# Performance work log

Hardware: AMD Instinct MI355X
Metric: run time of the kernel (lower is better)

Reference implementation:

```python
import jax, jax.numpy as jnp
import numpy as np

UNITS = 512
EPS = 1e-6

def setup_inputs() -> dict:
    key = jax.random.key(0)
    x = jax.random.normal(key, (262144, UNITS), dtype=jnp.float32)
    return {"x": x}

def reference(x):
    d = x.shape[1]
    # Gram matrix with diagonal jitter: [d, d]
    g = x.T @ x + jnp.eye(d, dtype=x.dtype) * EPS
    L = jnp.linalg.cholesky(g)  # lower triangular [d, d]
    # inv(L) via triangular solve (same math as tf.linalg.inv on L)
    L_inv = jax.scipy.linalg.solve_triangular(L, jnp.eye(d, dtype=x.dtype), lower=True)
    ortho_weights = L_inv.T * jnp.sqrt(jnp.float32(UNITS))
    return x @ ortho_weights
```

## Files before the change

kernel.cpp:

```cpp
#include <hip/hip_runtime.h>


#define EPSJ 1e-6f
#define SQRTD 22.627416997969522f

typedef short bf16x8 __attribute__((ext_vector_type(8)));
typedef float f32x4 __attribute__((ext_vector_type(4)));

__device__ __forceinline__ unsigned short f2bf(float f) {
  unsigned u = __float_as_uint(f);
  unsigned r = u + 0x7fffu + ((u >> 16) & 1u);
  return (unsigned short)(r >> 16);
}

__device__ __forceinline__ int swz(int row, int slot) {
  return slot ^ ((row ^ (row >> 3)) & 7);
}

__device__ __forceinline__ float wred(float s) {
  s += __shfl_xor(s, 1);  s += __shfl_xor(s, 2);  s += __shfl_xor(s, 4);
  s += __shfl_xor(s, 8);  s += __shfl_xor(s, 16); s += __shfl_xor(s, 32);
  return s;
}

#define GLOAD16(g, l)                                                         \
  __builtin_amdgcn_global_load_lds(                                           \
      (const __attribute__((address_space(1))) void*)(g),                     \
      (__attribute__((address_space(3))) void*)(l), 16, 0, 0)

__global__ void convert_bf(const float* __restrict__ X,
                           unsigned short* __restrict__ Xbf) {
  long idx = (long)blockIdx.x * blockDim.x + threadIdx.x;
  const long stride = (long)gridDim.x * blockDim.x;
  const long nch = 134217728 / 8;
  for (long i = idx; i < nch; i += stride) {
    float4 f0 = ((const float4*)X)[i * 2];
    float4 f1 = ((const float4*)X)[i * 2 + 1];
    uint4 o;
    o.x = (unsigned)f2bf(f0.x) | ((unsigned)f2bf(f0.y) << 16);
    o.y = (unsigned)f2bf(f0.z) | ((unsigned)f2bf(f0.w) << 16);
    o.z = (unsigned)f2bf(f1.x) | ((unsigned)f2bf(f1.y) << 16);
    o.w = (unsigned)f2bf(f1.z) | ((unsigned)f2bf(f1.w) << 16);
    ((uint4*)Xbf)[i] = o;
  }
}

__device__ __forceinline__ void stage_pack4(
    const unsigned short* __restrict__ src,
    unsigned short* dst, int c0, int kg) {
  uint4 r0 = *(const uint4*)src;
  uint4 r1 = *(const uint4*)(src + 512);
  uint4 r2 = *(const uint4*)(src + 1024);
  uint4 r3 = *(const uint4*)(src + 1536);
  unsigned a[4] = {r0.x, r0.y, r0.z, r0.w};
  unsigned b[4] = {r1.x, r1.y, r1.z, r1.w};
  unsigned c[4] = {r2.x, r2.y, r2.z, r2.w};
  unsigned d[4] = {r3.x, r3.y, r3.z, r3.w};
  const int khi = kg >> 1, koff = (kg & 1) * 8;
  #pragma unroll
  for (int s = 0; s < 8; ++s) {
    int wsel = s >> 1, sh = (s & 1) * 16;
    unsigned v0 = (a[wsel] >> sh) & 0xFFFFu;
    unsigned v1 = (b[wsel] >> sh) & 0xFFFFu;
    unsigned v2 = (c[wsel] >> sh) & 0xFFFFu;
    unsigned v3 = (d[wsel] >> sh) & 0xFFFFu;
    int cc = c0 + s;
    int sl = khi ^ ((cc ^ (cc >> 3)) & 7);
    *(uint2*)((char*)dst + cc * 128 + sl * 16 + koff) =
        make_uint2(v0 | (v1 << 16), v2 | (v3 << 16));
  }
}

__global__ __launch_bounds__(512, 2) void gram_bf(
    const unsigned short* __restrict__ Xbf, float* __restrict__ part,
    int nchunk) {
  __shared__ unsigned short As[256 * 64];
  __shared__ unsigned short Bs[256 * 64];
  const int b = blockIdx.x, pos = b % 3, chunk = b / 3;
  const int s0 = (int)((long)4096 * chunk / nchunk);
  const int s1 = (int)((long)4096 * (chunk + 1) / nchunk);
  const int ca = (pos == 1) ? 256 : 0;
  const int cb2 = (pos == 0) ? 0 : 256;
  const bool diag = (pos != 2);
  const int t = threadIdx.x, lane = t & 63, w = t >> 6;
  const int wr = w >> 2, wc = w & 3;

  f32x4 acc[8][4];
  const f32x4 zf = {0.f, 0.f, 0.f, 0.f};
  #pragma unroll
  for (int a = 0; a < 8; ++a)
    #pragma unroll
    for (int bb = 0; bb < 4; ++bb) acc[a][bb] = zf;

  const int c0 = (t & 31) * 8;
  const int kg = t >> 5;

  for (int ks = s0; ks < s1; ++ks) {
    long r = (long)ks * 64 + kg * 4;
    stage_pack4(Xbf + r * 512 + ca + c0, As, c0, kg);
    if (!diag) stage_pack4(Xbf + r * 512 + cb2 + c0, Bs, c0, kg);
    __syncthreads();
    const unsigned short* Bp = diag ? As : Bs;
    #pragma unroll
    for (int kk = 0; kk < 2; ++kk) {
      bf16x8 af[8], bfr[4];
      #pragma unroll
      for (int fm = 0; fm < 8; ++fm) {
        int row = wr * 128 + fm * 16 + (lane & 15);
        int slot = swz(row, kk * 4 + (lane >> 4));
        af[fm] = *(const bf16x8*)((const char*)As + row * 128 + slot * 16);
      }
      #pragma unroll
      for (int fn = 0; fn < 4; ++fn) {
        int row = wc * 64 + fn * 16 + (lane & 15);
        int slot = swz(row, kk * 4 + (lane >> 4));
        bfr[fn] = *(const bf16x8*)((const char*)Bp + row * 128 + slot * 16);
      }
      #pragma unroll
      for (int fm = 0; fm < 8; ++fm)
        #pragma unroll
        for (int fn = 0; fn < 4; ++fn)
          acc[fm][fn] = __builtin_amdgcn_mfma_f32_16x16x32_bf16(
              bfr[fn], af[fm], acc[fm][fn], 0, 0, 0);
    }
    __syncthreads();
  }
  float* out = part + (long)b * 65536;
  #pragma unroll
  for (int fm = 0; fm < 8; ++fm)
    #pragma unroll
    for (int fn = 0; fn < 4; ++fn) {
      int mi = wr * 128 + fm * 16 + (lane & 15);
      int nj = wc * 64 + fn * 16 + (lane >> 4) * 4;
      *(float4*)(out + mi * 256 + nj) = *(float4*)&acc[fm][fn];
    }
}

__global__ __launch_bounds__(512, 2) void gram_f32(
    const float* __restrict__ X, float* __restrict__ part, int nchunk) {
  __shared__ unsigned short As[256 * 64];
  __shared__ unsigned short Bs[256 * 64];
  const int b = blockIdx.x;
  const int pos = b % 3;
  const int chunk = b / 3;
  const int CR = 262144 / nchunk;
  const long r0 = (long)chunk * CR;
  const int ca = (pos == 1) ? 256 : 0;
  const int cb = (pos == 0) ? 0 : 256;
  const bool diag = (pos != 2);
  const int t = threadIdx.x, lane = t & 63, w = t >> 6;
  const int wr = w >> 2, wc = w & 3;

  f32x4 acc[8][4];
  const f32x4 zf = {0.f, 0.f, 0.f, 0.f};
  #pragma unroll
  for (int a = 0; a < 8; ++a)
    #pragma unroll
    for (int bb = 0; bb < 4; ++bb) acc[a][bb] = zf;

  const int c_oct = t & 31, msub = t >> 5;

  for (int ks = 0; ks < CR; ks += 64) {
    #pragma unroll
    for (int it = 0; it < 4; ++it) {
      int m = msub + 16 * it;
      long row = r0 + ks + m;
      const float4* sa = (const float4*)(X + row * 512 + ca + c_oct * 8);
      float4 a0 = sa[0], a1 = sa[1];
      {
        float v[8] = {a0.x, a0.y, a0.z, a0.w, a1.x, a1.y, a1.z, a1.w};
        #pragma unroll
        for (int s = 0; s < 8; ++s) {
          int c = c_oct * 8 + s;
          int off = c * 128 + ((2 * m) ^ (((c ^ (c >> 3)) & 7) << 4));
          *(unsigned short*)((char*)As + off) = f2bf(v[s]);
        }
      }
      if (!diag) {
        const float4* sb = (const float4*)(X + row * 512 + cb + c_oct * 8);
        float4 b0 = sb[0], b1 = sb[1];
        float v[8] = {b0.x, b0.y, b0.z, b0.w, b1.x, b1.y, b1.z, b1.w};
        #pragma unroll
        for (int s = 0; s < 8; ++s) {
          int c = c_oct * 8 + s;
          int off = c * 128 + ((2 * m) ^ (((c ^ (c >> 3)) & 7) << 4));
          *(unsigned short*)((char*)Bs + off) = f2bf(v[s]);
        }
      }
    }
    __syncthreads();
    const unsigned short* Bp = diag ? As : Bs;
    #pragma unroll
    for (int kk = 0; kk < 2; ++kk) {
      bf16x8 af[8], bfr[4];
      #pragma unroll
      for (int fm = 0; fm < 8; ++fm) {
        int row = wr * 128 + fm * 16 + (lane & 15);
        int slot = swz(row, kk * 4 + (lane >> 4));
        af[fm] = *(const bf16x8*)((const char*)As + row * 128 + slot * 16);
      }
      #pragma unroll
      for (int fn = 0; fn < 4; ++fn) {
        int row = wc * 64 + fn * 16 + (lane & 15);
        int slot = swz(row, kk * 4 + (lane >> 4));
        bfr[fn] = *(const bf16x8*)((const char*)Bp + row * 128 + slot * 16);
      }
      #pragma unroll
      for (int fm = 0; fm < 8; ++fm)
        #pragma unroll
        for (int fn = 0; fn < 4; ++fn)
          acc[fm][fn] = __builtin_amdgcn_mfma_f32_16x16x32_bf16(
              af[fm], bfr[fn], acc[fm][fn], 0, 0, 0);
    }
    __syncthreads();
  }
  float* out = part + (long)b * 65536;
  #pragma unroll
  for (int fm = 0; fm < 8; ++fm)
    #pragma unroll
    for (int fn = 0; fn < 4; ++fn)
      #pragma unroll
      for (int j = 0; j < 4; ++j) {
        int i  = wr * 128 + fm * 16 + (lane >> 4) * 4 + j;
        int jj = wc * 64 + fn * 16 + (lane & 15);
        out[i * 256 + jj] = acc[fm][fn][j];
      }
}

__global__ void gram_reduce(const float* __restrict__ part,
                            float* __restrict__ G, int nchunk) {
  int idx = blockIdx.x * 256 + threadIdx.x;
  int pos = idx >> 16;
  int e = idx & 65535;
  float s = 0.f;
  for (int ch = 0; ch < nchunk; ++ch)
    s += part[(long)(ch * 3 + pos) * 65536 + e];
  int i = e >> 8, j = e & 255;
  if (pos == 0) {
    G[i * 512 + j] = s;
  } else if (pos == 1) {
    G[(256 + i) * 512 + 256 + j] = s;
  } else {
    G[i * 512 + 256 + j] = s;
    G[(256 + j) * 512 + i] = s;
  }
}

__global__ __launch_bounds__(256) void chol_d64(float* __restrict__ G,
                                                float* __restrict__ Dinv,
                                                int p) {
  __shared__ float Pb[64][65];
  __shared__ float Sb[64][65];
  __shared__ float Inv[64][65];
  __shared__ float Tt[32][33];
  const int t = threadIdx.x;
  const int r0 = 64 * p;
  const int tr = (t >> 4) * 4, tc = (t & 15) * 4;

  for (int idx = t; idx < 4096; idx += 256) {
    int i = idx >> 6, j = idx & 63;
    float v = G[(long)(r0 + i) * 512 + r0 + j];
    if (i == j) v += EPSJ;
    Pb[i][j] = v;
  }
  __syncthreads();

  if (p > 0) {
    float cc[4][4] = {{0.f}};
    for (int r = 0; r < p; ++r) {
      for (int idx = t; idx < 4096; idx += 256) {
        int i = idx >> 6, j = idx & 63;
        Sb[i][j] = G[(long)(r0 + i) * 512 + 64 * r + j];
      }
      __syncthreads();
      #pragma unroll 4
      for (int k = 0; k < 64; ++k) {
        float a0 = Sb[tr][k], a1 = Sb[tr+1][k], a2 = Sb[tr+2][k], a3 = Sb[tr+3][k];
        float b0 = Sb[tc][k], b1 = Sb[tc+1][k], b2 = Sb[tc+2][k], b3 = Sb[tc+3][k];
        cc[0][0]+=a0*b0; cc[0][1]+=a0*b1; cc[0][2]+=a0*b2; cc[0][3]+=a0*b3;
        cc[1][0]+=a1*b0; cc[1][1]+=a1*b1; cc[1][2]+=a1*b2; cc[1][3]+=a1*b3;
        cc[2][0]+=a2*b0; cc[2][1]+=a2*b1; cc[2][2]+=a2*b2; cc[2][3]+=a2*b3;
        cc[3][0]+=a3*b0; cc[3][1]+=a3*b1; cc[3][2]+=a3*b2; cc[3][3]+=a3*b3;
      }
      __syncthreads();
    }
    #pragma unroll
    for (int u = 0; u < 4; ++u)
      #pragma unroll
      for (int v = 0; v < 4; ++v)
        Pb[tr + u][tc + v] -= cc[u][v];
    __syncthreads();
  }

  const int lane = t & 63, w = t >> 6;
  #pragma unroll
  for (int sp = 0; sp < 2; ++sp) {
    const int b0 = sp * 32;
    if (w == 0) {
      float rr[32];
      #pragma unroll
      for (int k = 0; k < 32; ++k)
        rr[k] = (lane < 32) ? Pb[b0 + lane][b0 + k] : 0.f;
      #pragma unroll
      for (int j = 0; j < 32; ++j) {
        float d = sqrtf(__shfl(rr[j], j));
        if (lane == j) rr[j] = d;
        else if (lane > j && lane < 32) rr[j] = rr[j] / d;
        float rj = rr[j];
        #pragma unroll
        for (int k = j + 1; k < 32; ++k) {
          float Lkj = __shfl(rj, k);
          if (lane > j && lane < 32) rr[k] -= rj * Lkj;
        }
      }
      #pragma unroll
      for (int k = 0; k < 32; ++k)
        if (lane < 32) Pb[b0 + lane][b0 + k] = rr[k];
    }
    __syncthreads();
    if (sp == 0) {
      if (t < 32) {
        int rw = 32 + t;
        float x[32];
        #pragma unroll
        for (int j = 0; j < 32; ++j) x[j] = Pb[rw][j];
        #pragma unroll
        for (int j = 0; j < 32; ++j) {
          float xj = x[j] / Pb[j][j];
          x[j] = xj;
          #pragma unroll
          for (int k2 = j + 1; k2 < 32; ++k2) x[k2] -= xj * Pb[k2][j];
        }
        #pragma unroll
        for (int j = 0; j < 32; ++j) Pb[rw][j] = x[j];
      }
      __syncthreads();
      {
        int i = 32 + (t >> 3), kb = 32 + (t & 7) * 4;
        float sv[4];
        #pragma unroll
        for (int e = 0; e < 4; ++e) sv[e] = Pb[i][kb + e];
        #pragma unroll 4
        for (int j = 0; j < 32; ++j) {
          float aij = Pb[i][j];
          #pragma unroll
          for (int e = 0; e < 4; ++e) sv[e] -= aij * Pb[kb + e][j];
        }
        #pragma unroll
        for (int e = 0; e < 4; ++e) Pb[i][kb + e] = sv[e];
      }
      __syncthreads();
    }
  }

  if (t < 64) {
    int col = t & 31, o = (t >> 5) * 32;
    float x[32];
    #pragma unroll
    for (int i = 0; i < 32; ++i) {
      float s = (i == col) ? 1.f : 0.f;
      #pragma unroll
      for (int j = 0; j < i; ++j) s -= Pb[o + i][o + j] * x[j];
      x[i] = s / Pb[o + i][o + i];
    }
    #pragma unroll
    for (int i = 0; i < 32; ++i) Inv[o + i][o + col] = x[i];
  }
  for (int idx = t; idx < 1024; idx += 256)
    Inv[idx >> 5][32 + (idx & 31)] = 0.f;
  __syncthreads();
  {
    int i = t >> 3, jb = (t & 7) * 4;
    float sv[4] = {0.f, 0.f, 0.f, 0.f};
    #pragma unroll 4
    for (int k = 0; k < 32; ++k) {
      float bik = Pb[32 + i][k];
      #pragma unroll
      for (int e = 0; e < 4; ++e) sv[e] += bik * Inv[k][jb + e];
    }
    #pragma unroll
    for (int e = 0; e < 4; ++e) Tt[i][jb + e] = sv[e];
  }
  __syncthreads();
  {
    int i = t >> 3, jb = (t & 7) * 4;
    float sv[4] = {0.f, 0.f, 0.f, 0.f};
    #pragma unroll 4
    for (int k = 0; k < 32; ++k) {
      float cik = Inv[32 + i][32 + k];
      #pragma unroll
      for (int e = 0; e < 4; ++e) sv[e] += cik * Tt[k][jb + e];
    }
    #pragma unroll
    for (int e = 0; e < 4; ++e) Inv[32 + i][jb + e] = -sv[e];
  }
  __syncthreads();
  for (int idx = t; idx < 4096; idx += 256) {
    int i = idx >> 6, j = idx & 63;
    G[(long)(r0 + i) * 512 + r0 + j] = Pb[i][j];
    Dinv[p * 4096 + idx] = Inv[i][j];
  }
}

__global__ __launch_bounds__(256) void chol_t64(float* __restrict__ G,
                                                const float* __restrict__ Dinv,
                                                int p) {
  __shared__ float SbI[64][65];
  __shared__ float SbP[64][65];
  __shared__ float Ub[64][65];
  __shared__ float Db[64][65];
  const int t = threadIdx.x;
  const long rI = 64 * (p + 1 + blockIdx.x), cP = 64 * p;
  const int tr = (t >> 4) * 4, tc = (t & 15) * 4;

  for (int idx = t; idx < 4096; idx += 256)
    Db[idx >> 6][idx & 63] = Dinv[p * 4096 + idx];

  float cc[4][4] = {{0.f}};
  for (int r = 0; r < p; ++r) {
    __syncthreads();
    for (int idx = t; idx < 4096; idx += 256) {
      int i = idx >> 6, j = idx & 63;
      SbI[i][j] = G[(rI + i) * 512 + 64 * r + j];
      SbP[i][j] = G[(cP + i) * 512 + 64 * r + j];
    }
    __syncthreads();
    #pragma unroll 4
    for (int k = 0; k < 64; ++k) {
      float a0 = SbI[tr][k], a1 = SbI[tr+1][k], a2 = SbI[tr+2][k], a3 = SbI[tr+3][k];
      float b0 = SbP[tc][k], b1 = SbP[tc+1][k], b2 = SbP[tc+2][k], b3 = SbP[tc+3][k];
      cc[0][0]+=a0*b0; cc[0][1]+=a0*b1; cc[0][2]+=a0*b2; cc[0][3]+=a0*b3;
      cc[1][0]+=a1*b0; cc[1][1]+=a1*b1; cc[1][2]+=a1*b2; cc[1][3]+=a1*b3;
      cc[2][0]+=a2*b0; cc[2][1]+=a2*b1; cc[2][2]+=a2*b2; cc[2][3]+=a2*b3;
      cc[3][0]+=a3*b0; cc[3][1]+=a3*b1; cc[3][2]+=a3*b2; cc[3][3]+=a3*b3;
    }
  }
  __syncthreads();
  #pragma unroll
  for (int u = 0; u < 4; ++u)
    #pragma unroll
    for (int v = 0; v < 4; ++v)
      Ub[tr + u][tc + v] =
          G[(rI + tr + u) * 512 + cP + tc + v] - cc[u][v];
  __syncthreads();
  float xx[4][4] = {{0.f}};
  #pragma unroll 4
  for (int k = 0; k < 64; ++k) {
    float a0 = Ub[tr][k], a1 = Ub[tr+1][k], a2 = Ub[tr+2][k], a3 = Ub[tr+3][k];
    float b0 = Db[tc][k], b1 = Db[tc+1][k], b2 = Db[tc+2][k], b3 = Db[tc+3][k];
    xx[0][0]+=a0*b0; xx[0][1]+=a0*b1; xx[0][2]+=a0*b2; xx[0][3]+=a0*b3;
    xx[1][0]+=a1*b0; xx[1][1]+=a1*b1; xx[1][2]+=a1*b2; xx[1][3]+=a1*b3;
    xx[2][0]+=a2*b0; xx[2][1]+=a2*b1; xx[2][2]+=a2*b2; xx[2][3]+=a2*b3;
    xx[3][0]+=a3*b0; xx[3][1]+=a3*b1; xx[3][2]+=a3*b2; xx[3][3]+=a3*b3;
  }
  #pragma unroll
  for (int u = 0; u < 4; ++u)
    #pragma unroll
    for (int v = 0; v < 4; ++v)
      G[(rI + tr + u) * 512 + cP + tc + v] = xx[u][v];
}

__global__ __launch_bounds__(256) void tri_assemble(
    const float* __restrict__ G, const float* __restrict__ Dinv,
    unsigned short* __restrict__ Wt) {
  __shared__ float Bsh[448 * 64];
  __shared__ float T[64 * 64];
  const int q = blockIdx.x, t = threadIdx.x;
  const int or_ = (t >> 4) * 4, oc = (t & 15) * 4;

  for (int p = q + 1; p < 8; ++p) {
    float cc[4][4] = {{0.f}};
    for (int r = q; r < p; ++r) {
      const float* Lbase = G + (long)(64 * p) * 512 + 64 * r;
      #pragma unroll 4
      for (int k = 0; k < 64; ++k) {
        float a0 = Lbase[(or_ + 0) * 512 + k];
        float a1 = Lbase[(or_ + 1) * 512 + k];
        float a2 = Lbase[(or_ + 2) * 512 + k];
        float a3 = Lbase[(or_ + 3) * 512 + k];
        float b0, b1, b2, b3;
        if (r == q) {
          const float* Bq = Dinv + q * 4096 + k * 64 + oc;
          b0 = Bq[0]; b1 = Bq[1]; b2 = Bq[2]; b3 = Bq[3];
        } else {
          const float* Br = Bsh + ((r - q - 1) * 64 + k) * 64 + oc;
          b0 = Br[0]; b1 = Br[1]; b2 = Br[2]; b3 = Br[3];
        }
        cc[0][0] += a0*b0; cc[0][1] += a0*b1; cc[0][2] += a0*b2; cc[0][3] += a0*b3;
        cc[1][0] += a1*b0; cc[1][1] += a1*b1; cc[1][2] += a1*b2; cc[1][3] += a1*b3;
        cc[2][0] += a2*b0; cc[2][1] += a2*b1; cc[2][2] += a2*b2; cc[2][3] += a2*b3;
        cc[3][0] += a3*b0; cc[3][1] += a3*b1; cc[3][2] += a3*b2; cc[3][3] += a3*b3;
      }
    }
    #pragma unroll
    for (int u = 0; u < 4; ++u)
      #pragma unroll
      for (int v = 0; v < 4; ++v)
        T[(or_ + u) * 64 + oc + v] = cc[u][v];
    __syncthreads();

    float c2[4][4] = {{0.f}};
    const float* Dp = Dinv + p * 4096;
    #pragma unroll 4
    for (int k = 0; k < 64; ++k) {
      float a0 = Dp[(or_ + 0) * 64 + k];
      float a1 = Dp[(or_ + 1) * 64 + k];
      float a2 = Dp[(or_ + 2) * 64 + k];
      float a3 = Dp[(or_ + 3) * 64 + k];
      const float* Tk = T + k * 64 + oc;
      float b0 = Tk[0], b1 = Tk[1], b2 = Tk[2], b3 = Tk[3];
      c2[0][0] += a0*b0; c2[0][1] += a0*b1; c2[0][2] += a0*b2; c2[0][3] += a0*b3;
      c2[1][0] += a1*b0; c2[1][1] += a1*b1; c2[1][2] += a1*b2; c2[1][3] += a1*b3;
      c2[2][0] += a2*b0; c2[2][1] += a2*b1; c2[2][2] += a2*b2; c2[2][3] += a2*b3;
      c2[3][0] += a3*b0; c2[3][1] += a3*b1; c2[3][2] += a3*b2; c2[3][3] += a3*b3;
    }
    #pragma unroll
    for (int u = 0; u < 4; ++u)
      #pragma unroll
      for (int v = 0; v < 4; ++v)
        Bsh[((p - q - 1) * 64 + or_ + u) * 64 + oc + v] = -c2[u][v];
    __syncthreads();
  }

  const int nr = (8 - q) * 64;
  for (int idx = t; idx < nr * 64; idx += 256) {
    int i = idx >> 6, kk = idx & 63;
    float v = (i < 64) ? Dinv[q * 4096 + i * 64 + kk]
                       : Bsh[(i - 64) * 64 + kk];
    int n = 64 * q + i;
    Wt[(long)n * 512 + 64 * q + kk] = f2bf(SQRTD * v);
  }
  for (int idx = t; idx < 64 * q * 64; idx += 256) {
    int n = idx >> 6, kk = idx & 63;
    Wt[(long)n * 512 + 64 * q + kk] = 0;
  }
}

__global__ void tri_inv(const float* __restrict__ G,
                        unsigned short* __restrict__ Wt) {
  int w = threadIdx.x >> 6, lane = threadIdx.x & 63;
  int c = blockIdx.x * 4 + w;
  float v8[8];
  #pragma unroll
  for (int q = 0; q < 8; ++q) v8[q] = 0.f;
  #pragma unroll
  for (int q = 0; q < 8; ++q) {
    for (int ii = 0; ii < 64; ++ii) {
      int i = q * 64 + ii;
      const float* Lrow = G + (long)i * 512;
      float s = 0.f;
      #pragma unroll
      for (int qq = 0; qq < 8; ++qq) {
        if (qq < q) s += v8[qq] * Lrow[qq * 64 + lane];
      }
      s += (lane < ii) ? v8[q] * Lrow[q * 64 + lane] : 0.f;
      s = wred(s);
      float xi = (((i == c) ? 1.f : 0.f) - s) / Lrow[i];
      if (lane == ii) v8[q] = xi;
    }
  }
  #pragma unroll
  for (int q = 0; q < 8; ++q) {
    int i = q * 64 + lane;
    Wt[(long)i * 512 + c] = f2bf(SQRTD * v8[q]);
  }
}

__global__ __launch_bounds__(512, 4) void ymm4(
    const unsigned short* __restrict__ Xbf,
    const unsigned short* __restrict__ Wt, float* __restrict__ Y) {
  __shared__ unsigned short As[2][128 * 64];
  __shared__ unsigned short Bs[2][128 * 64];
  const int t = threadIdx.x, lane = t & 63, w = t >> 6;
  const int id = blockIdx.x;
  const int xcd = id & 7, j = id >> 3;
  const long m0 = (long)((j >> 2) * 8 + xcd) * 128;
  const int n0 = (j & 3) * 128;
  const int wm = (w >> 1) * 32, wn = (w & 1) * 64;
  f32x4 acc[2][4];
  const f32x4 zf = {0.f, 0.f, 0.f, 0.f};
  #pragma unroll
  for (int a = 0; a < 2; ++a)
    #pragma unroll
    for (int bq = 0; bq < 4; ++bq) acc[a][bq] = zf;

  auto stage = [&](int buf, int k0) {
    #pragma unroll
    for (int h = 0; h < 2; ++h) {
      int seg = t + h * 512;
      int row = seg >> 3, sl = seg & 7;
      const unsigned short* sA =
          Xbf + (m0 + row) * 512 + k0 + swz(row, sl) * 8;
      const unsigned short* sB =
          Wt + (long)(n0 + row) * 512 + k0 + swz(row, sl) * 8;
      GLOAD16(sA, &As[buf][seg * 8]);
      GLOAD16(sB, &Bs[buf][seg * 8]);
    }
  };
  auto compute = [&](int buf) {
    #pragma unroll
    for (int kk = 0; kk < 2; ++kk) {
      bf16x8 af[2], bfr[4];
      #pragma unroll
      for (int fm = 0; fm < 2; ++fm) {
        int row = wm + fm * 16 + (lane & 15);
        af[fm] = *(const bf16x8*)((const char*)As[buf] + row * 128 +
                                  swz(row, kk * 4 + (lane >> 4)) * 16);
      }
      #pragma unroll
      for (int fn = 0; fn < 4; ++fn) {
        int row = wn + fn * 16 + (lane & 15);
        bfr[fn] = *(const bf16x8*)((const char*)Bs[buf] + row * 128 +
                                   swz(row, kk * 4 + (lane >> 4)) * 16);
      }
      #pragma unroll
      for (int fm = 0; fm < 2; ++fm)
        #pragma unroll
        for (int fn = 0; fn < 4; ++fn)
          acc[fm][fn] = __builtin_amdgcn_mfma_f32_16x16x32_bf16(
              bfr[fn], af[fm], acc[fm][fn], 0, 0, 0);
    }
  };

  stage(0, 0);
  __syncthreads();
  int cur = 0;
  #pragma unroll 1
  for (int kt = 0; kt < 7; ++kt) {
    stage(cur ^ 1, (kt + 1) * 64);
    compute(cur);
    __syncthreads();
    cur ^= 1;
  }
  compute(cur);

  #pragma unroll
  for (int fm = 0; fm < 2; ++fm)
    #pragma unroll
    for (int fn = 0; fn < 4; ++fn) {
      long row = m0 + wm + fm * 16 + (lane & 15);
      int col = n0 + wn + fn * 16 + (lane >> 4) * 4;
      *(float4*)(Y + row * 512 + col) = *(float4*)&acc[fm][fn];
    }
}

__global__ __launch_bounds__(256) void ymm_v1(const float* __restrict__ X,
                                              const unsigned short* __restrict__ Wt,
                                              float* __restrict__ Y) {
  __shared__ unsigned short As[128 * 64];
  __shared__ unsigned short Bs[128 * 64];
  const int t = threadIdx.x, lane = t & 63, w = t >> 6;
  const long m0 = (long)blockIdx.x * 128;
  const int n0 = blockIdx.y * 128;
  const int wm = (w >> 1) * 64, wn = (w & 1) * 64;
  f32x4 acc[4][4];
  const f32x4 zf = {0.f, 0.f, 0.f, 0.f};
  #pragma unroll
  for (int a = 0; a < 4; ++a)
    #pragma unroll
    for (int bq = 0; bq < 4; ++bq) acc[a][bq] = zf;
  const int ko = t & 7, mrow = t >> 3;

  for (int k0 = 0; k0 < 512; k0 += 64) {
    #pragma unroll
    for (int it = 0; it < 4; ++it) {
      int m = mrow + 32 * it;
      const float4* src = (const float4*)(X + (m0 + m) * 512 + k0 + ko * 8);
      float4 f0 = src[0], f1 = src[1];
      unsigned p0 = (unsigned)f2bf(f0.x) | ((unsigned)f2bf(f0.y) << 16);
      unsigned p1 = (unsigned)f2bf(f0.z) | ((unsigned)f2bf(f0.w) << 16);
      unsigned p2 = (unsigned)f2bf(f1.x) | ((unsigned)f2bf(f1.y) << 16);
      unsigned p3 = (unsigned)f2bf(f1.z) | ((unsigned)f2bf(f1.w) << 16);
      int slot = swz(m, ko);
      *(uint4*)((char*)As + m * 128 + slot * 16) = make_uint4(p0, p1, p2, p3);
    }
    #pragma unroll
    for (int it = 0; it < 4; ++it) {
      int n = mrow + 32 * it;
      uint4 raw = *(const uint4*)(Wt + (long)(n0 + n) * 512 + k0 + ko * 8);
      int slot = swz(n, ko);
      *(uint4*)((char*)Bs + n * 128 + slot * 16) = raw;
    }
    __syncthreads();
    #pragma unroll
    for (int kk = 0; kk < 2; ++kk) {
      bf16x8 af[4], bfr[4];
      #pragma unroll
      for (int fm = 0; fm < 4; ++fm) {
        int row = wm + fm * 16 + (lane & 15);
        af[fm] = *(const bf16x8*)((const char*)As + row * 128 +
                                  swz(row, kk * 4 + (lane >> 4)) * 16);
      }
      #pragma unroll
      for (int fn = 0; fn < 4; ++fn) {
        int row = wn + fn * 16 + (lane & 15);
        bfr[fn] = *(const bf16x8*)((const char*)Bs + row * 128 +
                                   swz(row, kk * 4 + (lane >> 4)) * 16);
      }
      #pragma unroll
      for (int fm = 0; fm < 4; ++fm)
        #pragma unroll
        for (int fn = 0; fn < 4; ++fn)
          acc[fm][fn] = __builtin_amdgcn_mfma_f32_16x16x32_bf16(
              af[fm], bfr[fn], acc[fm][fn], 0, 0, 0);
    }
    __syncthreads();
  }
  #pragma unroll
  for (int fm = 0; fm < 4; ++fm)
    #pragma unroll
    for (int fn = 0; fn < 4; ++fn)
      #pragma unroll
      for (int j = 0; j < 4; ++j) {
        long row = m0 + wm + fm * 16 + (lane >> 4) * 4 + j;
        int col = n0 + wn + fn * 16 + (lane & 15);
        Y[row * 512 + col] = acc[fm][fn][j];
      }
}

static void chol_chain(float* G, float* Dinv, hipStream_t stream) {
  for (int p = 0; p < 8; ++p) {
    chol_d64<<<1, 256, 0, stream>>>(G, Dinv, p);
    if (p < 7) chol_t64<<<7 - p, 256, 0, stream>>>(G, Dinv, p);
  }
}

extern "C" void kernel_launch(void* const* d_in, const int* in_sizes, int n_in,
                              void* d_out, int out_size, void* d_ws, size_t ws_size,
                              hipStream_t stream) {
  const float* X = (const float*)d_in[0];
  float* Y = (float*)d_out;
  char* ws = (char*)d_ws;
  float* G = (float*)ws;
  unsigned short* Wt = (unsigned short*)(ws + (1 << 20));
  float* Dinv = (float*)(ws + (1 << 20) + (1 << 19));

  const int NCH_FAST = 85;
  size_t part_off = (size_t)(2 << 20);
  size_t part_bytes = (size_t)NCH_FAST * 3 * 65536 * 4;
  size_t xbf_off = part_off + part_bytes;
  size_t need = xbf_off + (size_t)134217728 * 2;

  if (ws_size >= need) {
    float* part = (float*)(ws + part_off);
    unsigned short* Xbf = (unsigned short*)(ws + xbf_off);
    convert_bf<<<2048, 256, 0, stream>>>(X, Xbf);
    gram_bf<<<3 * NCH_FAST, 512, 0, stream>>>(Xbf, part, NCH_FAST);
    gram_reduce<<<768, 256, 0, stream>>>(part, G, NCH_FAST);
    chol_chain(G, Dinv, stream);
    tri_assemble<<<8, 256, 0, stream>>>(G, Dinv, Wt);
    ymm4<<<8192, 512, 0, stream>>>(Xbf, Wt, Y);
  } else {
    float* part = (float*)(ws + part_off);
    size_t fixed = part_off;
    int nchunk = 64;
    while (nchunk > 1 && fixed + (size_t)nchunk * 3 * 65536 * 4 > ws_size)
      nchunk >>= 1;
    gram_f32<<<3 * nchunk, 512, 0, stream>>>(X, part, nchunk);
    gram_reduce<<<768, 256, 0, stream>>>(part, G, nchunk);
    chol_chain(G, Dinv, stream);
    tri_inv<<<128, 256, 0, stream>>>(G, Wt);
    ymm_v1<<<dim3(2048, 4), 256, 0, stream>>>(X, Wt, Y);
  }
}
```

Baseline: 1.413 ms.

## Fuse bf16 conversion into off-diagonal Gram kernel and merge Cholesky launches

The standalone fp32-to-bf16 conversion pass is folded into a new Gram kernel that reads fp32 X, writes Xbf and computes the off-diagonal 256x256 block in the same pass. A second kernel then computes the two diagonal blocks from Xbf, and the chunk count rises from 85 to 255. The Cholesky diagonal-factor and trailing-update kernels merge into one launch per panel, where every block recomputes the diagonal factor redundantly, halving the serial launch count. The Y GEMM pipeline replaces __syncthreads with partial vmcnt waits and raw barriers to overlap loads with compute. The fallback path also switches to tri_assemble.

Result: slower. 1.581 ms (+11.9%).

```diff
diff --git a/kernel.cpp b/kernel.cpp
--- a/kernel.cpp
+++ b/kernel.cpp
@@ -17,37 +17,101 @@
   return slot ^ ((row ^ (row >> 3)) & 7);
 }
 
-__device__ __forceinline__ float wred(float s) {
-  s += __shfl_xor(s, 1);  s += __shfl_xor(s, 2);  s += __shfl_xor(s, 4);
-  s += __shfl_xor(s, 8);  s += __shfl_xor(s, 16); s += __shfl_xor(s, 32);
-  return s;
-}
-
 #define GLOAD16(g, l)                                                         \
   __builtin_amdgcn_global_load_lds(                                           \
       (const __attribute__((address_space(1))) void*)(g),                     \
       (__attribute__((address_space(3))) void*)(l), 16, 0, 0)
 
-__global__ void convert_bf(const float* __restrict__ X,
-                           unsigned short* __restrict__ Xbf) {
-  long idx = (long)blockIdx.x * blockDim.x + threadIdx.x;
-  const long stride = (long)gridDim.x * blockDim.x;
-  const long nch = 134217728 / 8;
-  for (long i = idx; i < nch; i += stride) {
-    float4 f0 = ((const float4*)X)[i * 2];
-    float4 f1 = ((const float4*)X)[i * 2 + 1];
-    uint4 o;
-    o.x = (unsigned)f2bf(f0.x) | ((unsigned)f2bf(f0.y) << 16);
-    o.y = (unsigned)f2bf(f0.z) | ((unsigned)f2bf(f0.w) << 16);
-    o.z = (unsigned)f2bf(f1.x) | ((unsigned)f2bf(f1.y) << 16);
-    o.w = (unsigned)f2bf(f1.z) | ((unsigned)f2bf(f1.w) << 16);
-    ((uint4*)Xbf)[i] = o;
-  }
+__global__ __launch_bounds__(512, 2) void gram_k1(
+    const float* __restrict__ X, unsigned short* __restrict__ Xbf,
+    float* __restrict__ part, int nchunk) {
+  __shared__ unsigned short As[256 * 64];
+  __shared__ unsigned short Bs[256 * 64];
+  const int b = blockIdx.x;
+  const int s0 = (int)((long)4096 * b / nchunk);
+  const int s1 = (int)((long)4096 * (b + 1) / nchunk);
+  const int t = threadIdx.x, lane = t & 63, w = t >> 6;
+  const int wr = w >> 2, wc = w & 3;
+  const int kg = t >> 6;
+  const int c = t & 63;
+  unsigned short* half = (c < 32) ? As : Bs;
+  const int cl = (c & 31) * 8;
+
+  f32x4 acc[8][4];
+  const f32x4 zf = {0.f, 0.f, 0.f, 0.f};
+  #pragma unroll
+  for (int a = 0; a < 8; ++a)
+    #pragma unroll
+    for (int bb = 0; bb < 4; ++bb) acc[a][bb] = zf;
+
+  for (int ks = s0; ks < s1; ++ks) {
+    long r0 = (long)ks * 64 + kg * 8;
+    const float* src = X + r0 * 512 + c * 8;
+    uint4 rp[8];
+    #pragma unroll
+    for (int rr = 0; rr < 8; ++rr) {
+      float4 f0 = *(const float4*)(src + rr * 512);
+      float4 f1 = *(const float4*)(src + rr * 512 + 4);
+      rp[rr].x = (unsigned)f2bf(f0.x) | ((unsigned)f2bf(f0.y) << 16);
+      rp[rr].y = (unsigned)f2bf(f0.z) | ((unsigned)f2bf(f0.w) << 16);
+      rp[rr].z = (unsigned)f2bf(f1.x) | ((unsigned)f2bf(f1.y) << 16);
+      rp[rr].w = (unsigned)f2bf(f1.z) | ((unsigned)f2bf(f1.w) << 16);
+      *(uint4*)(Xbf + (r0 + rr) * 512 + c * 8) = rp[rr];
+    }
+    #pragma unroll
+    for (int s = 0; s < 8; ++s) {
+      unsigned v[8];
+      #pragma unroll
+      for (int rr = 0; rr < 8; ++rr) {
+        unsigned word = (s & 4) ? ((s & 2) ? rp[rr].w : rp[rr].z)
+                                : ((s & 2) ? rp[rr].y : rp[rr].x);
+        v[rr] = (s & 1) ? (word >> 16) : (word & 0xFFFFu);
+      }
+      uint4 o = make_uint4(v[0] | (v[1] << 16), v[2] | (v[3] << 16),
+                           v[4] | (v[5] << 16), v[6] | (v[7] << 16));
+      int cc = cl + s;
+      int sl = kg ^ ((cc ^ (cc >> 3)) & 7);
+      *(uint4*)((char*)half + cc * 128 + sl * 16) = o;
+    }
+    __syncthreads();
+    #pragma unroll
+    for (int kk = 0; kk < 2; ++kk) {
+      bf16x8 af[8], bfr[4];
+      #pragma unroll
+      for (int fm = 0; fm < 8; ++fm) {
+        int row = wr * 128 + fm * 16 + (lane & 15);
+        af[fm] = *(const bf16x8*)((const char*)As + row * 128 +
+                                  swz(row, kk * 4 + (lane >> 4)) * 16);
+      }
+      #pragma unroll
+      for (int fn = 0; fn < 4; ++fn) {
+        int row = wc * 64 + fn * 16 + (lane & 15);
+        bfr[fn] = *(const bf16x8*)((const char*)Bs + row * 128 +
+                                   swz(row, kk * 4 + (lane >> 4)) * 16);
+      }
+      #pragma unroll
+      for (int fm = 0; fm < 8; ++fm)
+        #pragma unroll
+        for (int fn = 0; fn < 4; ++fn)
+          acc[fm][fn] = __builtin_amdgcn_mfma_f32_16x16x32_bf16(
+              bfr[fn], af[fm], acc[fm][fn], 0, 0, 0);
+    }
+    __syncthreads();
+  }
+  float* out = part + (long)(b * 3 + 2) * 65536;
+  #pragma unroll
+  for (int fm = 0; fm < 8; ++fm)
+    #pragma unroll
+    for (int fn = 0; fn < 4; ++fn) {
+      int mi = wr * 128 + fm * 16 + (lane & 15);
+      int nj = wc * 64 + fn * 16 + (lane >> 4) * 4;
+      *(float4*)(out + mi * 256 + nj) = *(float4*)&acc[fm][fn];
+    }
 }
 
 __device__ __forceinline__ void stage_pack4(
-    const unsigned short* __restrict__ src,
-    unsigned short* dst, int c0, int kg) {
+    const unsigned short* __restrict__ src, unsigned short* dst, int c0,
+    int kg) {
   uint4 r0 = *(const uint4*)src;
   uint4 r1 = *(const uint4*)(src + 512);
   uint4 r2 = *(const uint4*)(src + 1024);
@@ -71,17 +135,14 @@
   }
 }
 
-__global__ __launch_bounds__(512, 2) void gram_bf(
+__global__ __launch_bounds__(512, 2) void gram_k2(
     const unsigned short* __restrict__ Xbf, float* __restrict__ part,
     int nchunk) {
   __shared__ unsigned short As[256 * 64];
-  __shared__ unsigned short Bs[256 * 64];
-  const int b = blockIdx.x, pos = b % 3, chunk = b / 3;
+  const int b = blockIdx.x, pos = b & 1, chunk = b >> 1;
   const int s0 = (int)((long)4096 * chunk / nchunk);
   const int s1 = (int)((long)4096 * (chunk + 1) / nchunk);
-  const int ca = (pos == 1) ? 256 : 0;
-  const int cb2 = (pos == 0) ? 0 : 256;
-  const bool diag = (pos != 2);
+  const int ca = pos ? 256 : 0;
   const int t = threadIdx.x, lane = t & 63, w = t >> 6;
   const int wr = w >> 2, wc = w & 3;
 
@@ -98,23 +159,21 @@
   for (int ks = s0; ks < s1; ++ks) {
     long r = (long)ks * 64 + kg * 4;
     stage_pack4(Xbf + r * 512 + ca + c0, As, c0, kg);
-    if (!diag) stage_pack4(Xbf + r * 512 + cb2 + c0, Bs, c0, kg);
-    __syncthreads();
-    const unsigned short* Bp = diag ? As : Bs;
+    __syncthreads();
     #pragma unroll
     for (int kk = 0; kk < 2; ++kk) {
       bf16x8 af[8], bfr[4];
       #pragma unroll
       for (int fm = 0; fm < 8; ++fm) {
         int row = wr * 128 + fm * 16 + (lane & 15);
-        int slot = swz(row, kk * 4 + (lane >> 4));
-        af[fm] = *(const bf16x8*)((const char*)As + row * 128 + slot * 16);
+        af[fm] = *(const bf16x8*)((const char*)As + row * 128 +
+                                  swz(row, kk * 4 + (lane >> 4)) * 16);
       }
       #pragma unroll
       for (int fn = 0; fn < 4; ++fn) {
         int row = wc * 64 + fn * 16 + (lane & 15);
-        int slot = swz(row, kk * 4 + (lane >> 4));
-        bfr[fn] = *(const bf16x8*)((const char*)Bp + row * 128 + slot * 16);
+        bfr[fn] = *(const bf16x8*)((const char*)As + row * 128 +
+                                   swz(row, kk * 4 + (lane >> 4)) * 16);
       }
       #pragma unroll
       for (int fm = 0; fm < 8; ++fm)
@@ -125,7 +184,7 @@
     }
     __syncthreads();
   }
-  float* out = part + (long)b * 65536;
+  float* out = part + (long)(chunk * 3 + pos) * 65536;
   #pragma unroll
   for (int fm = 0; fm < 8; ++fm)
     #pragma unroll
@@ -171,8 +230,8 @@
         float v[8] = {a0.x, a0.y, a0.z, a0.w, a1.x, a1.y, a1.z, a1.w};
         #pragma unroll
         for (int s = 0; s < 8; ++s) {
-          int c = c_oct * 8 + s;
-          int off = c * 128 + ((2 * m) ^ (((c ^ (c >> 3)) & 7) << 4));
+          int cc = c_oct * 8 + s;
+          int off = cc * 128 + ((2 * m) ^ (((cc ^ (cc >> 3)) & 7) << 4));
           *(unsigned short*)((char*)As + off) = f2bf(v[s]);
         }
       }
@@ -182,8 +241,8 @@
         float v[8] = {b0.x, b0.y, b0.z, b0.w, b1.x, b1.y, b1.z, b1.w};
         #pragma unroll
         for (int s = 0; s < 8; ++s) {
-          int c = c_oct * 8 + s;
-          int off = c * 128 + ((2 * m) ^ (((c ^ (c >> 3)) & 7) << 4));
+          int cc = c_oct * 8 + s;
+          int off = cc * 128 + ((2 * m) ^ (((cc ^ (cc >> 3)) & 7) << 4));
           *(unsigned short*)((char*)Bs + off) = f2bf(v[s]);
         }
       }
@@ -196,21 +255,21 @@
       #pragma unroll
       for (int fm = 0; fm < 8; ++fm) {
         int row = wr * 128 + fm * 16 + (lane & 15);
-        int slot = swz(row, kk * 4 + (lane >> 4));
-        af[fm] = *(const bf16x8*)((const char*)As + row * 128 + slot * 16);
+        af[fm] = *(const bf16x8*)((const char*)As + row * 128 +
+                                  swz(row, kk * 4 + (lane >> 4)) * 16);
       }
       #pragma unroll
       for (int fn = 0; fn < 4; ++fn) {
         int row = wc * 64 + fn * 16 + (lane & 15);
-        int slot = swz(row, kk * 4 + (lane >> 4));
-        bfr[fn] = *(const bf16x8*)((const char*)Bp + row * 128 + slot * 16);
+        bfr[fn] = *(const bf16x8*)((const char*)Bp + row * 128 +
+                                   swz(row, kk * 4 + (lane >> 4)) * 16);
       }
       #pragma unroll
       for (int fm = 0; fm < 8; ++fm)
         #pragma unroll
         for (int fn = 0; fn < 4; ++fn)
           acc[fm][fn] = __builtin_amdgcn_mfma_f32_16x16x32_bf16(
-              af[fm], bfr[fn], acc[fm][fn], 0, 0, 0);
+              bfr[fn], af[fm], acc[fm][fn], 0, 0, 0);
     }
     __syncthreads();
   }
@@ -218,13 +277,11 @@
   #pragma unroll
   for (int fm = 0; fm < 8; ++fm)
     #pragma unroll
-    for (int fn = 0; fn < 4; ++fn)
-      #pragma unroll
-      for (int j = 0; j < 4; ++j) {
-        int i  = wr * 128 + fm * 16 + (lane >> 4) * 4 + j;
-        int jj = wc * 64 + fn * 16 + (lane & 15);
-        out[i * 256 + jj] = acc[fm][fn][j];
-      }
+    for (int fn = 0; fn < 4; ++fn) {
+      int mi = wr * 128 + fm * 16 + (lane & 15);
+      int nj = wc * 64 + fn * 16 + (lane >> 4) * 4;
+      *(float4*)(out + mi * 256 + nj) = *(float4*)&acc[fm][fn];
+    }
 }
 
 __global__ void gram_reduce(const float* __restrict__ part,
@@ -246,12 +303,14 @@
   }
 }
 
-__global__ __launch_bounds__(256) void chol_d64(float* __restrict__ G,
-                                                float* __restrict__ Dinv,
-                                                int p) {
+__global__ __launch_bounds__(256) void chol_step(float* __restrict__ G,
+                                                 float* __restrict__ Dinv,
+                                                 int p) {
   __shared__ float Pb[64][65];
   __shared__ float Sb[64][65];
   __shared__ float Inv[64][65];
+  __shared__ float SbP[64][65];
+  __shared__ float Ub[64][65];
   __shared__ float Tt[32][33];
   const int t = threadIdx.x;
   const int r0 = 64 * p;
@@ -395,44 +454,31 @@
     for (int e = 0; e < 4; ++e) Inv[32 + i][jb + e] = -sv[e];
   }
   __syncthreads();
-  for (int idx = t; idx < 4096; idx += 256) {
-    int i = idx >> 6, j = idx & 63;
-    G[(long)(r0 + i) * 512 + r0 + j] = Pb[i][j];
-    Dinv[p * 4096 + idx] = Inv[i][j];
-  }
-}
-
-__global__ __launch_bounds__(256) void chol_t64(float* __restrict__ G,
-                                                const float* __restrict__ Dinv,
-                                                int p) {
-  __shared__ float SbI[64][65];
-  __shared__ float SbP[64][65];
-  __shared__ float Ub[64][65];
-  __shared__ float Db[64][65];
-  const int t = threadIdx.x;
-  const long rI = 64 * (p + 1 + blockIdx.x), cP = 64 * p;
-  const int tr = (t >> 4) * 4, tc = (t & 15) * 4;
-
-  for (int idx = t; idx < 4096; idx += 256)
-    Db[idx >> 6][idx & 63] = Dinv[p * 4096 + idx];
-
-  float cc[4][4] = {{0.f}};
+
+  if (blockIdx.x == 0) {
+    for (int idx = t; idx < 4096; idx += 256)
+      Dinv[p * 4096 + idx] = Inv[idx >> 6][idx & 63];
+    return;
+  }
+
+  const long rI = 64 * (p + blockIdx.x), cP = 64 * p;
+  float cc2[4][4] = {{0.f}};
   for (int r = 0; r < p; ++r) {
     __syncthreads();
     for (int idx = t; idx < 4096; idx += 256) {
       int i = idx >> 6, j = idx & 63;
-      SbI[i][j] = G[(rI + i) * 512 + 64 * r + j];
+      Sb[i][j] = G[(rI + i) * 512 + 64 * r + j];
       SbP[i][j] = G[(cP + i) * 512 + 64 * r + j];
     }
     __syncthreads();
     #pragma unroll 4
     for (int k = 0; k < 64; ++k) {
-      float a0 = SbI[tr][k], a1 = SbI[tr+1][k], a2 = SbI[tr+2][k], a3 = SbI[tr+3][k];
+      float a0 = Sb[tr][k], a1 = Sb[tr+1][k], a2 = Sb[tr+2][k], a3 = Sb[tr+3][k];
       float b0 = SbP[tc][k], b1 = SbP[tc+1][k], b2 = SbP[tc+2][k], b3 = SbP[tc+3][k];
-      cc[0][0]+=a0*b0; cc[0][1]+=a0*b1; cc[0][2]+=a0*b2; cc[0][3]+=a0*b3;
-      cc[1][0]+=a1*b0; cc[1][1]+=a1*b1; cc[1][2]+=a1*b2; cc[1][3]+=a1*b3;
-      cc[2][0]+=a2*b0; cc[2][1]+=a2*b1; cc[2][2]+=a2*b2; cc[2][3]+=a2*b3;
-      cc[3][0]+=a3*b0; cc[3][1]+=a3*b1; cc[3][2]+=a3*b2; cc[3][3]+=a3*b3;
+      cc2[0][0]+=a0*b0; cc2[0][1]+=a0*b1; cc2[0][2]+=a0*b2; cc2[0][3]+=a0*b3;
+      cc2[1][0]+=a1*b0; cc2[1][1]+=a1*b1; cc2[1][2]+=a1*b2; cc2[1][3]+=a1*b3;
+      cc2[2][0]+=a2*b0; cc2[2][1]+=a2*b1; cc2[2][2]+=a2*b2; cc2[2][3]+=a2*b3;
+      cc2[3][0]+=a3*b0; cc2[3][1]+=a3*b1; cc2[3][2]+=a3*b2; cc2[3][3]+=a3*b3;
     }
   }
   __syncthreads();
@@ -440,14 +486,13 @@
   for (int u = 0; u < 4; ++u)
     #pragma unroll
     for (int v = 0; v < 4; ++v)
-      Ub[tr + u][tc + v] =
-          G[(rI + tr + u) * 512 + cP + tc + v] - cc[u][v];
+      Ub[tr + u][tc + v] = G[(rI + tr + u) * 512 + cP + tc + v] - cc2[u][v];
   __syncthreads();
   float xx[4][4] = {{0.f}};
   #pragma unroll 4
   for (int k = 0; k < 64; ++k) {
     float a0 = Ub[tr][k], a1 = Ub[tr+1][k], a2 = Ub[tr+2][k], a3 = Ub[tr+3][k];
-    float b0 = Db[tc][k], b1 = Db[tc+1][k], b2 = Db[tc+2][k], b3 = Db[tc+3][k];
+    float b0 = Inv[tc][k], b1 = Inv[tc+1][k], b2 = Inv[tc+2][k], b3 = Inv[tc+3][k];
     xx[0][0]+=a0*b0; xx[0][1]+=a0*b1; xx[0][2]+=a0*b2; xx[0][3]+=a0*b3;
     xx[1][0]+=a1*b0; xx[1][1]+=a1*b1; xx[1][2]+=a1*b2; xx[1][3]+=a1*b3;
     xx[2][0]+=a2*b0; xx[2][1]+=a2*b1; xx[2][2]+=a2*b2; xx[2][3]+=a2*b3;
@@ -536,37 +581,7 @@
   }
 }
 
-__global__ void tri_inv(const float* __restrict__ G,
-                        unsigned short* __restrict__ Wt) {
-  int w = threadIdx.x >> 6, lane = threadIdx.x & 63;
-  int c = blockIdx.x * 4 + w;
-  float v8[8];
-  #pragma unroll
-  for (int q = 0; q < 8; ++q) v8[q] = 0.f;
-  #pragma unroll
-  for (int q = 0; q < 8; ++q) {
-    for (int ii = 0; ii < 64; ++ii) {
-      int i = q * 64 + ii;
-      const float* Lrow = G + (long)i * 512;
-      float s = 0.f;
-      #pragma unroll
-      for (int qq = 0; qq < 8; ++qq) {
-        if (qq < q) s += v8[qq] * Lrow[qq * 64 + lane];
-      }
-      s += (lane < ii) ? v8[q] * Lrow[q * 64 + lane] : 0.f;
-      s = wred(s);
-      float xi = (((i == c) ? 1.f : 0.f) - s) / Lrow[i];
-      if (lane == ii) v8[q] = xi;
-    }
-  }
-  #pragma unroll
-  for (int q = 0; q < 8; ++q) {
-    int i = q * 64 + lane;
-    Wt[(long)i * 512 + c] = f2bf(SQRTD * v8[q]);
-  }
-}
-
-__global__ __launch_bounds__(512, 4) void ymm4(
+__global__ __launch_bounds__(512, 4) void ymm5(
     const unsigned short* __restrict__ Xbf,
     const unsigned short* __restrict__ Wt, float* __restrict__ Y) {
   __shared__ unsigned short As[2][128 * 64];
@@ -623,15 +638,22 @@
   };
 
   stage(0, 0);
-  __syncthreads();
+  asm volatile("s_waitcnt vmcnt(0)" ::: "memory");
+  __builtin_amdgcn_s_barrier();
   int cur = 0;
   #pragma unroll 1
   for (int kt = 0; kt < 7; ++kt) {
     stage(cur ^ 1, (kt + 1) * 64);
+    asm volatile("s_waitcnt vmcnt(4)" ::: "memory");
+    __builtin_amdgcn_sched_barrier(0);
+    __builtin_amdgcn_s_barrier();
     compute(cur);
-    __syncthreads();
+    __builtin_amdgcn_s_barrier();
     cur ^= 1;
   }
+  asm volatile("s_waitcnt vmcnt(0)" ::: "memory");
+  __builtin_amdgcn_sched_barrier(0);
+  __builtin_amdgcn_s_barrier();
   compute(cur);
 
   #pragma unroll
@@ -718,13 +740,6 @@
       }
 }
 
-static void chol_chain(float* G, float* Dinv, hipStream_t stream) {
-  for (int p = 0; p < 8; ++p) {
-    chol_d64<<<1, 256, 0, stream>>>(G, Dinv, p);
-    if (p < 7) chol_t64<<<7 - p, 256, 0, stream>>>(G, Dinv, p);
-  }
-}
-
 extern "C" void kernel_launch(void* const* d_in, const int* in_sizes, int n_in,
                               void* d_out, int out_size, void* d_ws, size_t ws_size,
                               hipStream_t stream) {
@@ -735,21 +750,22 @@
   unsigned short* Wt = (unsigned short*)(ws + (1 << 20));
   float* Dinv = (float*)(ws + (1 << 20) + (1 << 19));
 
-  const int NCH_FAST = 85;
+  const int NCH = 255;
   size_t part_off = (size_t)(2 << 20);
-  size_t part_bytes = (size_t)NCH_FAST * 3 * 65536 * 4;
+  size_t part_bytes = (size_t)NCH * 3 * 65536 * 4;
   size_t xbf_off = part_off + part_bytes;
   size_t need = xbf_off + (size_t)134217728 * 2;
 
   if (ws_size >= need) {
     float* part = (float*)(ws + part_off);
     unsigned short* Xbf = (unsigned short*)(ws + xbf_off);
-    convert_bf<<<2048, 256, 0, stream>>>(X, Xbf);
-    gram_bf<<<3 * NCH_FAST, 512, 0, stream>>>(Xbf, part, NCH_FAST);
-    gram_reduce<<<768, 256, 0, stream>>>(part, G, NCH_FAST);
-    chol_chain(G, Dinv, stream);
+    gram_k1<<<NCH, 512, 0, stream>>>(X, Xbf, part, NCH);
+    gram_k2<<<2 * NCH, 512, 0, stream>>>(Xbf, part, NCH);
+    gram_reduce<<<768, 256, 0, stream>>>(part, G, NCH);
+    for (int p = 0; p < 8; ++p)
+      chol_step<<<8 - p, 256, 0, stream>>>(G, Dinv, p);
     tri_assemble<<<8, 256, 0, stream>>>(G, Dinv, Wt);
-    ymm4<<<8192, 512, 0, stream>>>(Xbf, Wt, Y);
+    ymm5<<<8192, 512, 0, stream>>>(Xbf, Wt, Y);
   } else {
     float* part = (float*)(ws + part_off);
     size_t fixed = part_off;
@@ -758,8 +774,9 @@
       nchunk >>= 1;
     gram_f32<<<3 * nchunk, 512, 0, stream>>>(X, part, nchunk);
     gram_reduce<<<768, 256, 0, stream>>>(part, G, nchunk);
-    chol_chain(G, Dinv, stream);
-    tri_inv<<<128, 256, 0, stream>>>(G, Wt);
+    for (int p = 0; p < 8; ++p)
+      chol_step<<<8 - p, 256, 0, stream>>>(G, Dinv, p);
+    tri_assemble<<<8, 256, 0, stream>>>(G, Dinv, Wt);
     ymm_v1<<<dim3(2048, 4), 256, 0, stream>>>(X, Wt, Y);
   }
 }
```

## Shrink final GEMM N-tile to 64, raise occupancy, vectorize gram partial stores

Applied to the files above, without the earlier changes.

The final Y = Xbf·Wt kernel now uses 128x64 output tiles instead of 128x128, launches twice as many blocks, and targets 6 blocks per CU through launch bounds, which halves the B-operand LDS footprint. The gram kernel swaps its MFMA operand order so each lane holds four consecutive columns, letting partial-sum stores go out as float4 instead of scalar writes. The slow fallback path's tri_inv is replaced by the blocked tri_assemble. The smaller tile means X tiles are re-read from global/L2 more often, in exchange for more waves in flight to hide latency.

Result: no change. 1.429 ms (+1.2%).

```diff
diff --git a/kernel.cpp b/kernel.cpp
--- a/kernel.cpp
+++ b/kernel.cpp
@@ -171,8 +171,8 @@
         float v[8] = {a0.x, a0.y, a0.z, a0.w, a1.x, a1.y, a1.z, a1.w};
         #pragma unroll
         for (int s = 0; s < 8; ++s) {
-          int c = c_oct * 8 + s;
-          int off = c * 128 + ((2 * m) ^ (((c ^ (c >> 3)) & 7) << 4));
+          int cc = c_oct * 8 + s;
+          int off = cc * 128 + ((2 * m) ^ (((cc ^ (cc >> 3)) & 7) << 4));
           *(unsigned short*)((char*)As + off) = f2bf(v[s]);
         }
       }
@@ -182,8 +182,8 @@
         float v[8] = {b0.x, b0.y, b0.z, b0.w, b1.x, b1.y, b1.z, b1.w};
         #pragma unroll
         for (int s = 0; s < 8; ++s) {
-          int c = c_oct * 8 + s;
-          int off = c * 128 + ((2 * m) ^ (((c ^ (c >> 3)) & 7) << 4));
+          int cc = c_oct * 8 + s;
+          int off = cc * 128 + ((2 * m) ^ (((cc ^ (cc >> 3)) & 7) << 4));
           *(unsigned short*)((char*)Bs + off) = f2bf(v[s]);
         }
       }
@@ -210,7 +210,7 @@
         #pragma unroll
         for (int fn = 0; fn < 4; ++fn)
           acc[fm][fn] = __builtin_amdgcn_mfma_f32_16x16x32_bf16(
-              af[fm], bfr[fn], acc[fm][fn], 0, 0, 0);
+              bfr[fn], af[fm], acc[fm][fn], 0, 0, 0);
     }
     __syncthreads();
   }
@@ -218,13 +218,11 @@
   #pragma unroll
   for (int fm = 0; fm < 8; ++fm)
     #pragma unroll
-    for (int fn = 0; fn < 4; ++fn)
-      #pragma unroll
-      for (int j = 0; j < 4; ++j) {
-        int i  = wr * 128 + fm * 16 + (lane >> 4) * 4 + j;
-        int jj = wc * 64 + fn * 16 + (lane & 15);
-        out[i * 256 + jj] = acc[fm][fn][j];
-      }
+    for (int fn = 0; fn < 4; ++fn) {
+      int mi = wr * 128 + fm * 16 + (lane & 15);
+      int nj = wc * 64 + fn * 16 + (lane >> 4) * 4;
+      *(float4*)(out + mi * 256 + nj) = *(float4*)&acc[fm][fn];
+    }
 }
 
 __global__ void gram_reduce(const float* __restrict__ part,
@@ -536,53 +534,23 @@
   }
 }
 
-__global__ void tri_inv(const float* __restrict__ G,
-                        unsigned short* __restrict__ Wt) {
-  int w = threadIdx.x >> 6, lane = threadIdx.x & 63;
-  int c = blockIdx.x * 4 + w;
-  float v8[8];
-  #pragma unroll
-  for (int q = 0; q < 8; ++q) v8[q] = 0.f;
-  #pragma unroll
-  for (int q = 0; q < 8; ++q) {
-    for (int ii = 0; ii < 64; ++ii) {
-      int i = q * 64 + ii;
-      const float* Lrow = G + (long)i * 512;
-      float s = 0.f;
-      #pragma unroll
-      for (int qq = 0; qq < 8; ++qq) {
-        if (qq < q) s += v8[qq] * Lrow[qq * 64 + lane];
-      }
-      s += (lane < ii) ? v8[q] * Lrow[q * 64 + lane] : 0.f;
-      s = wred(s);
-      float xi = (((i == c) ? 1.f : 0.f) - s) / Lrow[i];
-      if (lane == ii) v8[q] = xi;
-    }
-  }
-  #pragma unroll
-  for (int q = 0; q < 8; ++q) {
-    int i = q * 64 + lane;
-    Wt[(long)i * 512 + c] = f2bf(SQRTD * v8[q]);
-  }
-}
-
-__global__ __launch_bounds__(512, 4) void ymm4(
+__global__ __launch_bounds__(512, 6) void ymm6(
     const unsigned short* __restrict__ Xbf,
     const unsigned short* __restrict__ Wt, float* __restrict__ Y) {
   __shared__ unsigned short As[2][128 * 64];
-  __shared__ unsigned short Bs[2][128 * 64];
+  __shared__ unsigned short Bs[2][64 * 64];
   const int t = threadIdx.x, lane = t & 63, w = t >> 6;
   const int id = blockIdx.x;
   const int xcd = id & 7, j = id >> 3;
-  const long m0 = (long)((j >> 2) * 8 + xcd) * 128;
-  const int n0 = (j & 3) * 128;
-  const int wm = (w >> 1) * 32, wn = (w & 1) * 64;
-  f32x4 acc[2][4];
+  const long m0 = (long)((j >> 3) * 8 + xcd) * 128;
+  const int n0 = (j & 7) * 64;
+  const int wm = (w >> 1) * 32, wn = (w & 1) * 32;
+  f32x4 acc[2][2];
   const f32x4 zf = {0.f, 0.f, 0.f, 0.f};
   #pragma unroll
   for (int a = 0; a < 2; ++a)
     #pragma unroll
-    for (int bq = 0; bq < 4; ++bq) acc[a][bq] = zf;
+    for (int bq = 0; bq < 2; ++bq) acc[a][bq] = zf;
 
   auto stage = [&](int buf, int k0) {
     #pragma unroll
@@ -591,16 +559,19 @@
       int row = seg >> 3, sl = seg & 7;
       const unsigned short* sA =
           Xbf + (m0 + row) * 512 + k0 + swz(row, sl) * 8;
+      GLOAD16(sA, &As[buf][seg * 8]);
+    }
+    {
+      int row = t >> 3, sl = t & 7;
       const unsigned short* sB =
           Wt + (long)(n0 + row) * 512 + k0 + swz(row, sl) * 8;
-      GLOAD16(sA, &As[buf][seg * 8]);
-      GLOAD16(sB, &Bs[buf][seg * 8]);
+      GLOAD16(sB, &Bs[buf][t * 8]);
     }
   };
   auto compute = [&](int buf) {
     #pragma unroll
     for (int kk = 0; kk < 2; ++kk) {
-      bf16x8 af[2], bfr[4];
+      bf16x8 af[2], bfr[2];
       #pragma unroll
       for (int fm = 0; fm < 2; ++fm) {
         int row = wm + fm * 16 + (lane & 15);
@@ -608,7 +579,7 @@
                                   swz(row, kk * 4 + (lane >> 4)) * 16);
       }
       #pragma unroll
-      for (int fn = 0; fn < 4; ++fn) {
+      for (int fn = 0; fn < 2; ++fn) {
         int row = wn + fn * 16 + (lane & 15);
         bfr[fn] = *(const bf16x8*)((const char*)Bs[buf] + row * 128 +
                                    swz(row, kk * 4 + (lane >> 4)) * 16);
@@ -616,7 +587,7 @@
       #pragma unroll
       for (int fm = 0; fm < 2; ++fm)
         #pragma unroll
-        for (int fn = 0; fn < 4; ++fn)
+        for (int fn = 0; fn < 2; ++fn)
           acc[fm][fn] = __builtin_amdgcn_mfma_f32_16x16x32_bf16(
               bfr[fn], af[fm], acc[fm][fn], 0, 0, 0);
     }
@@ -637,7 +608,7 @@
   #pragma unroll
   for (int fm = 0; fm < 2; ++fm)
     #pragma unroll
-    for (int fn = 0; fn < 4; ++fn) {
+    for (int fn = 0; fn < 2; ++fn) {
       long row = m0 + wm + fm * 16 + (lane & 15);
       int col = n0 + wn + fn * 16 + (lane >> 4) * 4;
       *(float4*)(Y + row * 512 + col) = *(float4*)&acc[fm][fn];
@@ -749,7 +720,7 @@
     gram_reduce<<<768, 256, 0, stream>>>(part, G, NCH_FAST);
     chol_chain(G, Dinv, stream);
     tri_assemble<<<8, 256, 0, stream>>>(G, Dinv, Wt);
-    ymm4<<<8192, 512, 0, stream>>>(Xbf, Wt, Y);
+    ymm6<<<16384, 512, 0, stream>>>(Xbf, Wt, Y);
   } else {
     float* part = (float*)(ws + part_off);
     size_t fixed = part_off;
@@ -759,7 +730,7 @@
     gram_f32<<<3 * nchunk, 512, 0, stream>>>(X, part, nchunk);
     gram_reduce<<<768, 256, 0, stream>>>(part, G, nchunk);
     chol_chain(G, Dinv, stream);
-    tri_inv<<<128, 256, 0, stream>>>(G, Wt);
+    tri_assemble<<<8, 256, 0, stream>>>(G, Dinv, Wt);
     ymm_v1<<<dim3(2048, 4), 256, 0, stream>>>(X, Wt, Y);
   }
 }
```
